# Optimization experiments

Hardware: AMD Instinct MI355X
Metric: run time of the kernel (lower is better)

## Reference

```python
import jax, jax.numpy as jnp
import numpy as np

B, T, C, H, D = 2, 2048, 1024, 16, 64

def setup_inputs() -> dict:
    key = jax.random.key(0)
    ks = jax.random.split(key, 5)
    s = 1.0 / np.sqrt(C)
    return {
        "hidden_states": jax.random.normal(ks[0], (B, T, C), jnp.float32),
        "Wq": jax.random.normal(ks[1], (H, C, D), jnp.float32) * s,
        "Wk": jax.random.normal(ks[2], (H, C, D), jnp.float32) * s,
        "Wv": jax.random.normal(ks[3], (H, C, D), jnp.float32) * s,
        "Wo": jax.random.normal(ks[4], (C, C), jnp.float32) * s,
    }

def reference(hidden_states, Wq, Wk, Wv, Wo):
    x = hidden_states  # (B, T, C)
    q = jnp.einsum("btc,hcd->bhtd", x, Wq)
    k = jnp.einsum("btc,hcd->bhtd", x, Wk)
    v = jnp.einsum("btc,hcd->bhtd", x, Wv)
    scale = 1.0 / jnp.sqrt(jnp.asarray(D, x.dtype))
    scores = jnp.einsum("bhtd,bhsd->bhts", q, k) * scale  # (B,H,T,T)
    Tlen = x.shape[1]
    causal = jnp.tril(jnp.ones((Tlen, Tlen), bool))
    scores = jnp.where(causal, scores, jnp.asarray(-jnp.inf, x.dtype))
    probs = jax.nn.softmax(scores, axis=-1)
    heads = jnp.einsum("bhts,bhsd->bhtd", probs, v)  # (B,H,T,D)
    concat = heads.transpose(0, 2, 1, 3).reshape(x.shape[0], Tlen, H * D)  # (B,T,C)
    return jnp.einsum("btc,oc->bto", concat, Wo)  # output projection (dropout=0)
```

## Files before the change

### kernel.cpp

```cpp
#include <hip/hip_runtime.h>
#include <math.h>

#define B_ 2
#define T_ 2048
#define C_ 1024
#define H_ 16
#define D_ 64

typedef short short8 __attribute__((ext_vector_type(8)));
typedef float f32x4 __attribute__((ext_vector_type(4)));
typedef float f32x16 __attribute__((ext_vector_type(16)));

#define LOG2E 1.44269504088896f

__device__ __forceinline__ unsigned short f2bf(float f) {
    unsigned int u = __float_as_uint(f);
    u += 0x7FFFu + ((u >> 16) & 1u);
    return (unsigned short)(u >> 16);
}

#define NCAST 2560

__global__ __launch_bounds__(256) void prep_all(
    const float* __restrict__ x,  const float* __restrict__ Wq,
    const float* __restrict__ Wk, const float* __restrict__ Wv,
    const float* __restrict__ Wo,
    unsigned short* __restrict__ xb,   unsigned short* __restrict__ Wall,
    unsigned short* __restrict__ wob,  int nX, int nW)
{
    const int bid = blockIdx.x;
    const int tid = threadIdx.x;
    if (bid < NCAST) {
        int i = (bid * 256 + tid) * 8;
        const float* s;
        unsigned short* d;
        if (i < nX) { s = x + i; d = xb + i; }
        else {
            int j = i - nX;
            if (j >= nW) return;
            s = Wo + j; d = wob + j;
        }
        float4 a = *(const float4*)s;
        float4 b = *(const float4*)(s + 4);
        ushort4 o0, o1;
        o0.x = f2bf(a.x); o0.y = f2bf(a.y); o0.z = f2bf(a.z); o0.w = f2bf(a.w);
        o1.x = f2bf(b.x); o1.y = f2bf(b.y); o1.z = f2bf(b.z); o1.w = f2bf(b.w);
        *(ushort4*)d = o0;
        *(ushort4*)(d + 4) = o1;
        return;
    }
    __shared__ float t[64][65];
    const int tb = bid - NCAST;
    const int c0 = (tb & 15) * 64;
    const int h  = (tb >> 4) & 15;
    const int z  = tb >> 8;
    const float* W = (z == 0) ? Wq : (z == 1) ? Wk : Wv;
    unsigned short* Wt = Wall + (size_t)z * H_ * D_ * C_;
    const int r = tid >> 4, c4 = (tid & 15) * 4;
    #pragma unroll
    for (int p = 0; p < 4; p++) {
        int cl = r + p * 16;
        float4 v = *(const float4*)&W[((size_t)h * C_ + c0 + cl) * D_ + c4];
        t[cl][c4 + 0] = v.x; t[cl][c4 + 1] = v.y;
        t[cl][c4 + 2] = v.z; t[cl][c4 + 3] = v.w;
    }
    __syncthreads();
    #pragma unroll
    for (int p = 0; p < 4; p++) {
        int d = r + p * 16;
        ushort4 o;
        o.x = f2bf(t[c4 + 0][d]); o.y = f2bf(t[c4 + 1][d]);
        o.z = f2bf(t[c4 + 2][d]); o.w = f2bf(t[c4 + 3][d]);
        *(ushort4*)&Wt[((size_t)h * D_ + d) * C_ + c0 + c4] = o;
    }
}

__global__ __launch_bounds__(256) void qkv_big(
    const unsigned short* __restrict__ X,
    const unsigned short* __restrict__ Wall,
    unsigned short* __restrict__ Qo,
    unsigned short* __restrict__ Ko,
    unsigned short* __restrict__ Vt)
{
    __shared__ unsigned short As[128][72];
    __shared__ unsigned short Bs[128][72];

    const int m0 = blockIdx.x * 128;
    const int n0 = blockIdx.y * 128;
    const int z  = n0 >> 10;
    const int tid = threadIdx.x;
    const int w = tid >> 6, lane = tid & 63, quad = lane >> 4, l16 = lane & 15;
    const int wm = w & 1, wn = w >> 1;
    const int lrow = tid >> 3, lcol = (tid & 7) * 8;

    f32x4 acc[4][4] = {};

    short8 ar[4], br[4];
    #pragma unroll
    for (int p = 0; p < 4; p++) {
        int r = lrow + p * 32;
        ar[p] = *(const short8*)&X[(size_t)(m0 + r) * C_ + lcol];
        br[p] = *(const short8*)&Wall[(size_t)(n0 + r) * C_ + lcol];
    }

    for (int k0 = 0; k0 < C_; k0 += 64) {
        __syncthreads();
        #pragma unroll
        for (int p = 0; p < 4; p++) {
            int r = lrow + p * 32;
            *(short8*)&As[r][lcol] = ar[p];
            *(short8*)&Bs[r][lcol] = br[p];
        }
        __syncthreads();
        if (k0 + 64 < C_) {
            #pragma unroll
            for (int p = 0; p < 4; p++) {
                int r = lrow + p * 32;
                ar[p] = *(const short8*)&X[(size_t)(m0 + r) * C_ + k0 + 64 + lcol];
                br[p] = *(const short8*)&Wall[(size_t)(n0 + r) * C_ + k0 + 64 + lcol];
            }
        }
        #pragma unroll
        for (int ks = 0; ks < 2; ks++) {
            short8 af[4], bf[4];
            #pragma unroll
            for (int i = 0; i < 4; i++)
                af[i] = *(const short8*)&As[wm * 64 + i * 16 + l16][ks * 32 + quad * 8];
            #pragma unroll
            for (int j = 0; j < 4; j++)
                bf[j] = *(const short8*)&Bs[wn * 64 + j * 16 + l16][ks * 32 + quad * 8];
            #pragma unroll
            for (int i = 0; i < 4; i++)
                #pragma unroll
                for (int j = 0; j < 4; j++)
                    acc[i][j] = __builtin_amdgcn_mfma_f32_16x16x32_bf16(af[i], bf[j], acc[i][j], 0, 0, 0);
        }
    }

    if (z == 2) {
        #pragma unroll
        for (int j = 0; j < 4; j++) {
            const int n = n0 + wn * 64 + j * 16 + l16;
            const int h = (n >> 6) & 15, d = n & 63;
            #pragma unroll
            for (int i = 0; i < 4; i++) {
                const int m = m0 + wm * 64 + i * 16 + quad * 4;
                const int b = m >> 11, t = m & (T_ - 1);
                ushort4 pk;
                pk.x = f2bf(acc[i][j][0]);
                pk.y = f2bf(acc[i][j][1]);
                pk.z = f2bf(acc[i][j][2]);
                pk.w = f2bf(acc[i][j][3]);
                *(ushort4*)&Vt[(((size_t)b * H_ + h) * D_ + d) * T_ + t] = pk;
            }
        }
    } else {
        const float scale = (z == 0) ? 0.125f * LOG2E : 1.0f;
        unsigned short* O = (z == 0) ? Qo : Ko;
        #pragma unroll
        for (int j = 0; j < 4; j++) {
            const int n = n0 + wn * 64 + j * 16 + l16;
            const int h = (n >> 6) & 15, d = n & 63;
            #pragma unroll
            for (int i = 0; i < 4; i++)
                #pragma unroll
                for (int r = 0; r < 4; r++) {
                    const int m = m0 + wm * 64 + i * 16 + quad * 4 + r;
                    const int b = m >> 11, t = m & (T_ - 1);
                    O[(((size_t)b * H_ + h) * T_ + t) * D_ + d] = f2bf(acc[i][j][r] * scale);
                }
        }
    }
}

__global__ __launch_bounds__(512, 4) void flash_mfma(
    const unsigned short* __restrict__ Q,
    const unsigned short* __restrict__ K,
    const unsigned short* __restrict__ Vt,
    unsigned short* __restrict__ CC)
{
    __shared__ unsigned short kst[64][72];
    __shared__ unsigned short vts[64][72];
    __shared__ float fob[2][64][68];
    __shared__ float flb_p[2][64];
    __shared__ float flb_t[2][64];

    const int dd   = blockIdx.x;
    const int xs   = dd & 7;
    const int loc  = dd >> 3;
    const int half = loc >> 5, li = loc & 31;
    const int hsub = li & 3, pr = li >> 2;
    const int p    = half ? (15 - pr) : pr;
    const int head = xs * 4 + hsub;
    const int h = head & 15, b = head >> 4;

    const int tid = threadIdx.x;
    const int w = tid >> 6, lane = tid & 63;
    const int l31 = lane & 31, hi = lane >> 5;
    const int wg = w & 3;
    const int g  = w >> 2;
    const int sw = (wg & 1) * 32;
    const int qw = (wg >> 1) * 32;
    const int lrow = tid >> 3, lcol = (tid & 7) * 8;
    const size_t hb  = ((size_t)b * H_ + h) * T_;
    const size_t hbD = ((size_t)b * H_ + h) * D_;

    const int qb  = g ? (31 - p) : p;
    const int q0  = qb * 64;
    const int myn = qb + 1;
    const int nkb = 32 - p;

    short8 qf[4];
    #pragma unroll
    for (int k4 = 0; k4 < 4; k4++)
        qf[k4] = *(const short8*)&Q[(hb + q0 + qw + l31) * D_ + k4 * 16 + hi * 8];

    float l_lane = 0.0f;
    f32x16 o0 = {}, o1 = {};

    short8 kreg, vreg;
    kreg = *(const short8*)&K[(hb + lrow) * D_ + lcol];
    vreg = *(const short8*)&Vt[(hbD + lrow) * T_ + lcol];

    for (int kb = 0; kb < nkb; kb++) {
        __syncthreads();
        *(short8*)&kst[lrow][lcol] = kreg;
        *(short8*)&vts[lrow][lcol] = vreg;
        __syncthreads();
        if (kb + 1 < nkb) {
            const int k0n = (kb + 1) * 64;
            kreg = *(const short8*)&K[(hb + k0n + lrow) * D_ + lcol];
            vreg = *(const short8*)&Vt[(hbD + lrow) * T_ + k0n + lcol];
        }

        if (kb < myn) {
            f32x16 S = {};
            __builtin_amdgcn_s_setprio(1);
            #pragma unroll
            for (int k4 = 0; k4 < 4; k4++) {
                short8 kf = *(const short8*)&kst[sw + l31][k4 * 16 + hi * 8];
                S = __builtin_amdgcn_mfma_f32_32x32x16_bf16(kf, qf[k4], S, 0, 0, 0);
            }
            __builtin_amdgcn_s_setprio(0);

            if (kb == qb) {
                #pragma unroll
                for (int reg = 0; reg < 16; reg++) {
                    const int srel = (reg & 3) + 4 * hi + 8 * (reg >> 2);
                    if (sw + srel > qw + l31) S[reg] = -INFINITY;
                }
            }

            unsigned Wd[8];
            #pragma unroll
            for (int blk = 0; blk < 4; blk++) {
                float e0 = exp2f(S[4 * blk + 0]);
                float e1 = exp2f(S[4 * blk + 1]);
                float e2 = exp2f(S[4 * blk + 2]);
                float e3 = exp2f(S[4 * blk + 3]);
                l_lane += (e0 + e1) + (e2 + e3);
                Wd[2 * blk + 0] = __builtin_amdgcn_perm(
                    __float_as_uint(e1) + 0x8000u, __float_as_uint(e0) + 0x8000u, 0x07060302u);
                Wd[2 * blk + 1] = __builtin_amdgcn_perm(
                    __float_as_uint(e3) + 0x8000u, __float_as_uint(e2) + 0x8000u, 0x07060302u);
            }

            unsigned a0 = Wd[0], b0 = Wd[2];
            asm("v_permlane32_swap_b32 %0, %1" : "+v"(a0), "+v"(b0));
            unsigned a1 = Wd[1], b1 = Wd[3];
            asm("v_permlane32_swap_b32 %0, %1" : "+v"(a1), "+v"(b1));
            unsigned c0 = Wd[4], d0 = Wd[6];
            asm("v_permlane32_swap_b32 %0, %1" : "+v"(c0), "+v"(d0));
            unsigned c1 = Wd[5], d1 = Wd[7];
            asm("v_permlane32_swap_b32 %0, %1" : "+v"(c1), "+v"(d1));
            union { unsigned u[4]; short8 v; } pw0, pw1;
            pw0.u[0] = a0; pw0.u[1] = a1; pw0.u[2] = b0; pw0.u[3] = b1;
            pw1.u[0] = c0; pw1.u[1] = c1; pw1.u[2] = d0; pw1.u[3] = d1;

            __builtin_amdgcn_s_setprio(1);
            {
                short8 vf;
                vf = *(const short8*)&vts[l31][sw + hi * 8];
                o0 = __builtin_amdgcn_mfma_f32_32x32x16_bf16(pw0.v, vf, o0, 0, 0, 0);
                vf = *(const short8*)&vts[l31][sw + 16 + hi * 8];
                o0 = __builtin_amdgcn_mfma_f32_32x32x16_bf16(pw1.v, vf, o0, 0, 0, 0);
                vf = *(const short8*)&vts[32 + l31][sw + hi * 8];
                o1 = __builtin_amdgcn_mfma_f32_32x32x16_bf16(pw0.v, vf, o1, 0, 0, 0);
                vf = *(const short8*)&vts[32 + l31][sw + 16 + hi * 8];
                o1 = __builtin_amdgcn_mfma_f32_32x32x16_bf16(pw1.v, vf, o1, 0, 0, 0);
            }
            __builtin_amdgcn_s_setprio(0);
        }
    }

    l_lane += __shfl_xor(l_lane, 32);

    if (wg & 1) {
        if (lane < 32) flb_p[g][qw + lane] = l_lane;
        #pragma unroll
        for (int reg = 0; reg < 16; reg++) {
            const int qr = (reg & 3) + 4 * hi + 8 * (reg >> 2);
            fob[g][qw + qr][l31]      = o0[reg];
            fob[g][qw + qr][32 + l31] = o1[reg];
        }
    }
    __syncthreads();
    if (!(wg & 1)) {
        const float lt = l_lane + flb_p[g][qw + l31];
        if (lane < 32) flb_t[g][qw + lane] = lt;
        #pragma unroll
        for (int reg = 0; reg < 16; reg++) {
            const int qr = (reg & 3) + 4 * hi + 8 * (reg >> 2);
            const float invl = 1.0f / flb_t[g][qw + qr];
            const float v0 = o0[reg] + fob[g][qw + qr][l31];
            const float v1 = o1[reg] + fob[g][qw + qr][32 + l31];
            const int t = q0 + qw + qr;
            CC[((size_t)b * T_ + t) * C_ + h * D_ + l31]      = f2bf(v0 * invl);
            CC[((size_t)b * T_ + t) * C_ + h * D_ + 32 + l31] = f2bf(v1 * invl);
        }
    }
}

__global__ __launch_bounds__(256) void out_big(
    const unsigned short* __restrict__ X,
    const unsigned short* __restrict__ Wob,
    float* __restrict__ out)
{
    __shared__ unsigned short As[128][72];
    __shared__ unsigned short Bs[128][72];

    const int m0 = blockIdx.x * 128;
    const int n0 = blockIdx.y * 128;
    const int tid = threadIdx.x;
    const int w = tid >> 6, lane = tid & 63, quad = lane >> 4, l16 = lane & 15;
    const int wm = w & 1, wn = w >> 1;
    const int lrow = tid >> 3, lcol = (tid & 7) * 8;

    f32x4 acc[4][4] = {};

    short8 ar[4], br[4];
    #pragma unroll
    for (int p = 0; p < 4; p++) {
        int r = lrow + p * 32;
        ar[p] = *(const short8*)&X[(size_t)(m0 + r) * C_ + lcol];
        br[p] = *(const short8*)&Wob[(size_t)(n0 + r) * C_ + lcol];
    }

    for (int k0 = 0; k0 < C_; k0 += 64) {
        __syncthreads();
        #pragma unroll
        for (int p = 0; p < 4; p++) {
            int r = lrow + p * 32;
            *(short8*)&As[r][lcol] = ar[p];
            *(short8*)&Bs[r][lcol] = br[p];
        }
        __syncthreads();
        if (k0 + 64 < C_) {
            #pragma unroll
            for (int p = 0; p < 4; p++) {
                int r = lrow + p * 32;
                ar[p] = *(const short8*)&X[(size_t)(m0 + r) * C_ + k0 + 64 + lcol];
                br[p] = *(const short8*)&Wob[(size_t)(n0 + r) * C_ + k0 + 64 + lcol];
            }
        }
        #pragma unroll
        for (int ks = 0; ks < 2; ks++) {
            short8 af[4], bf[4];
            #pragma unroll
            for (int i = 0; i < 4; i++)
                af[i] = *(const short8*)&As[wm * 64 + i * 16 + l16][ks * 32 + quad * 8];
            #pragma unroll
            for (int j = 0; j < 4; j++)
                bf[j] = *(const short8*)&Bs[wn * 64 + j * 16 + l16][ks * 32 + quad * 8];
            #pragma unroll
            for (int i = 0; i < 4; i++)
                #pragma unroll
                for (int j = 0; j < 4; j++)
                    acc[i][j] = __builtin_amdgcn_mfma_f32_16x16x32_bf16(af[i], bf[j], acc[i][j], 0, 0, 0);
        }
    }

    #pragma unroll
    for (int i = 0; i < 4; i++)
        #pragma unroll
        for (int j = 0; j < 4; j++)
            #pragma unroll
            for (int r = 0; r < 4; r++)
                out[(size_t)(m0 + wm * 64 + i * 16 + quad * 4 + r) * C_ + n0 + wn * 64 + j * 16 + l16] = acc[i][j][r];
}

extern "C" void kernel_launch(void* const* d_in, const int* in_sizes, int n_in,
                              void* d_out, int out_size, void* d_ws, size_t ws_size,
                              hipStream_t stream) {
    const float* x  = (const float*)d_in[0];
    const float* Wq = (const float*)d_in[1];
    const float* Wk = (const float*)d_in[2];
    const float* Wv = (const float*)d_in[3];
    const float* Wo = (const float*)d_in[4];
    float* out = (float*)d_out;

    const size_t nX = (size_t)B_ * T_ * C_;
    const size_t nW = (size_t)H_ * C_ * D_;
    const size_t nQ = (size_t)B_ * H_ * T_ * D_;
    unsigned short* xb   = (unsigned short*)d_ws;
    unsigned short* Wall = xb + nX;
    unsigned short* Wob  = Wall + 3 * nW;
    unsigned short* Qb   = Wob + nW;
    unsigned short* Kb   = Qb + nQ;
    unsigned short* Vtb  = Kb + nQ;
    unsigned short* CCb  = Vtb + nQ;

    prep_all<<<dim3(NCAST + 768), 256, 0, stream>>>(
        x, Wq, Wk, Wv, Wo, xb, Wall, Wob, (int)nX, (int)nW);
    qkv_big<<<dim3(32, 24), 256, 0, stream>>>(xb, Wall, Qb, Kb, Vtb);
    flash_mfma<<<dim3(512), 512, 0, stream>>>(Qb, Kb, Vtb, CCb);
    out_big<<<dim3(32, 8), 256, 0, stream>>>(CCb, Wob, out);
}
```

Baseline: 172.4 us.

## Rebalance causal flash workload between warp groups by splitting key blocks

The two 4-wave groups in each flash block previously handled a short query block p and a long query block 31-p, so group 0 idled for most of the loop. Now group 0 finishes its short block, switches to the long query block, and both groups process alternating key blocks, with two K/V tiles staged per step. Partial outputs and row sums are merged through shared memory in staged reductions at the end. This adds shared memory, extra register loads and more barriers in exchange for a shorter critical path per block.

Result: slower. 206.5 us (+19.8%).

```diff
diff --git a/kernel.cpp b/kernel.cpp
--- a/kernel.cpp
+++ b/kernel.cpp
@@ -179,8 +179,8 @@
     const unsigned short* __restrict__ Vt,
     unsigned short* __restrict__ CC)
 {
-    __shared__ unsigned short kst[64][72];
-    __shared__ unsigned short vts[64][72];
+    __shared__ unsigned short kst[128][72];
+    __shared__ unsigned short vts[128][72];
     __shared__ float fob[2][64][68];
     __shared__ float flb_p[2][64];
     __shared__ float flb_t[2][64];
@@ -205,45 +205,103 @@
     const size_t hb  = ((size_t)b * H_ + h) * T_;
     const size_t hbD = ((size_t)b * H_ + h) * D_;
 
-    const int qb  = g ? (31 - p) : p;
-    const int q0  = qb * 64;
-    const int myn = qb + 1;
-    const int nkb = 32 - p;
+    const int qbB = 31 - p;
+    const int p2s = p + 2;
+
+    int myqb = g ? qbB : p;
 
     short8 qf[4];
     #pragma unroll
     for (int k4 = 0; k4 < 4; k4++)
-        qf[k4] = *(const short8*)&Q[(hb + q0 + qw + l31) * D_ + k4 * 16 + hi * 8];
+        qf[k4] = *(const short8*)&Q[(hb + myqb * 64 + qw + l31) * D_ + k4 * 16 + hi * 8];
 
     float l_lane = 0.0f;
     f32x16 o0 = {}, o1 = {};
 
-    short8 kreg, vreg;
+    short8 kreg, vreg, kreg2, vreg2;
     kreg = *(const short8*)&K[(hb + lrow) * D_ + lcol];
     vreg = *(const short8*)&Vt[(hbD + lrow) * T_ + lcol];
 
-    for (int kb = 0; kb < nkb; kb++) {
+    for (int it = 0; it <= 16; it++) {
         __syncthreads();
         *(short8*)&kst[lrow][lcol] = kreg;
         *(short8*)&vts[lrow][lcol] = vreg;
+        if (it >= p2s) {
+            *(short8*)&kst[64 + lrow][lcol] = kreg2;
+            *(short8*)&vts[64 + lrow][lcol] = vreg2;
+        }
         __syncthreads();
-        if (kb + 1 < nkb) {
-            const int k0n = (kb + 1) * 64;
-            kreg = *(const short8*)&K[(hb + k0n + lrow) * D_ + lcol];
-            vreg = *(const short8*)&Vt[(hbD + lrow) * T_ + k0n + lcol];
-        }
-
-        if (kb < myn) {
+        if (it < 16) {
+            const int nit = it + 1;
+            if (nit < p2s) {
+                const int k0n = nit * 64;
+                kreg = *(const short8*)&K[(hb + k0n + lrow) * D_ + lcol];
+                vreg = *(const short8*)&Vt[(hbD + lrow) * T_ + k0n + lcol];
+            } else {
+                const int k0a = (p2s + 2 * (nit - p2s)) * 64;
+                kreg  = *(const short8*)&K[(hb + k0a + lrow) * D_ + lcol];
+                vreg  = *(const short8*)&Vt[(hbD + lrow) * T_ + k0a + lcol];
+                kreg2 = *(const short8*)&K[(hb + k0a + 64 + lrow) * D_ + lcol];
+                vreg2 = *(const short8*)&Vt[(hbD + lrow) * T_ + k0a + 64 + lcol];
+            }
+        }
+
+        if (g == 0 && it == p + 1) {
+            float lr = l_lane + __shfl_xor(l_lane, 32);
+            if (sw) {
+                if (lane < 32) flb_p[0][qw + lane] = lr;
+                #pragma unroll
+                for (int reg = 0; reg < 16; reg++) {
+                    const int qr = (reg & 3) + 4 * hi + 8 * (reg >> 2);
+                    fob[0][qw + qr][l31]      = o0[reg];
+                    fob[0][qw + qr][32 + l31] = o1[reg];
+                    o0[reg] = 0.0f; o1[reg] = 0.0f;
+                }
+                l_lane = 0.0f;
+            }
+            myqb = qbB;
+            #pragma unroll
+            for (int k4 = 0; k4 < 4; k4++)
+                qf[k4] = *(const short8*)&Q[(hb + qbB * 64 + qw + l31) * D_ + k4 * 16 + hi * 8];
+        }
+        if (g == 0 && !sw && it == p2s) {
+            float lr = l_lane + __shfl_xor(l_lane, 32);
+            float lt = lr + flb_p[0][qw + l31];
+            if (lane < 32) flb_t[0][qw + lane] = lt;
+            #pragma unroll
+            for (int reg = 0; reg < 16; reg++) {
+                const int qr = (reg & 3) + 4 * hi + 8 * (reg >> 2);
+                const float invl = 1.0f / flb_t[0][qw + qr];
+                const float v0 = o0[reg] + fob[0][qw + qr][l31];
+                const float v1 = o1[reg] + fob[0][qw + qr][32 + l31];
+                const int t = p * 64 + qw + qr;
+                CC[((size_t)b * T_ + t) * C_ + h * D_ + l31]      = f2bf(v0 * invl);
+                CC[((size_t)b * T_ + t) * C_ + h * D_ + 32 + l31] = f2bf(v1 * invl);
+                o0[reg] = 0.0f; o1[reg] = 0.0f;
+            }
+            l_lane = 0.0f;
+        }
+
+        bool active = true;
+        int kcur = it, rb = 0;
+        if (g == 0) {
+            if (it == p + 1)      active = false;
+            else if (it >= p2s)   kcur = p2s + 2 * (it - p2s);
+        } else {
+            if (it >= p2s)      { kcur = p2s + 2 * (it - p2s) + 1; rb = 64; }
+        }
+
+        if (active) {
             f32x16 S = {};
             __builtin_amdgcn_s_setprio(1);
             #pragma unroll
             for (int k4 = 0; k4 < 4; k4++) {
-                short8 kf = *(const short8*)&kst[sw + l31][k4 * 16 + hi * 8];
+                short8 kf = *(const short8*)&kst[rb + sw + l31][k4 * 16 + hi * 8];
                 S = __builtin_amdgcn_mfma_f32_32x32x16_bf16(kf, qf[k4], S, 0, 0, 0);
             }
             __builtin_amdgcn_s_setprio(0);
 
-            if (kb == qb) {
+            if (kcur == myqb) {
                 #pragma unroll
                 for (int reg = 0; reg < 16; reg++) {
                     const int srel = (reg & 3) + 4 * hi + 8 * (reg >> 2);
@@ -280,41 +338,81 @@
             __builtin_amdgcn_s_setprio(1);
             {
                 short8 vf;
-                vf = *(const short8*)&vts[l31][sw + hi * 8];
+                vf = *(const short8*)&vts[rb + l31][sw + hi * 8];
                 o0 = __builtin_amdgcn_mfma_f32_32x32x16_bf16(pw0.v, vf, o0, 0, 0, 0);
-                vf = *(const short8*)&vts[l31][sw + 16 + hi * 8];
+                vf = *(const short8*)&vts[rb + l31][sw + 16 + hi * 8];
                 o0 = __builtin_amdgcn_mfma_f32_32x32x16_bf16(pw1.v, vf, o0, 0, 0, 0);
-                vf = *(const short8*)&vts[32 + l31][sw + hi * 8];
+                vf = *(const short8*)&vts[rb + 32 + l31][sw + hi * 8];
                 o1 = __builtin_amdgcn_mfma_f32_32x32x16_bf16(pw0.v, vf, o1, 0, 0, 0);
-                vf = *(const short8*)&vts[32 + l31][sw + 16 + hi * 8];
+                vf = *(const short8*)&vts[rb + 32 + l31][sw + 16 + hi * 8];
                 o1 = __builtin_amdgcn_mfma_f32_32x32x16_bf16(pw1.v, vf, o1, 0, 0, 0);
             }
             __builtin_amdgcn_s_setprio(0);
         }
     }
 
-    l_lane += __shfl_xor(l_lane, 32);
-
-    if (wg & 1) {
-        if (lane < 32) flb_p[g][qw + lane] = l_lane;
+    __syncthreads();
+    if (g == 1 && sw) {
+        float lr = l_lane + __shfl_xor(l_lane, 32);
+        if (lane < 32) flb_p[1][qw + lane] = lr;
         #pragma unroll
         for (int reg = 0; reg < 16; reg++) {
             const int qr = (reg & 3) + 4 * hi + 8 * (reg >> 2);
-            fob[g][qw + qr][l31]      = o0[reg];
-            fob[g][qw + qr][32 + l31] = o1[reg];
-        }
-    }
-    __syncthreads();
-    if (!(wg & 1)) {
-        const float lt = l_lane + flb_p[g][qw + l31];
-        if (lane < 32) flb_t[g][qw + lane] = lt;
+            fob[1][qw + qr][l31]      = o0[reg];
+            fob[1][qw + qr][32 + l31] = o1[reg];
+        }
+    }
+    if (g == 0 && !sw && p == 15) {
+        float lr = l_lane + __shfl_xor(l_lane, 32);
+        float lt = lr + flb_p[0][qw + l31];
+        if (lane < 32) flb_t[0][qw + lane] = lt;
         #pragma unroll
         for (int reg = 0; reg < 16; reg++) {
             const int qr = (reg & 3) + 4 * hi + 8 * (reg >> 2);
-            const float invl = 1.0f / flb_t[g][qw + qr];
-            const float v0 = o0[reg] + fob[g][qw + qr][l31];
-            const float v1 = o1[reg] + fob[g][qw + qr][32 + l31];
-            const int t = q0 + qw + qr;
+            const float invl = 1.0f / flb_t[0][qw + qr];
+            const float v0 = o0[reg] + fob[0][qw + qr][l31];
+            const float v1 = o1[reg] + fob[0][qw + qr][32 + l31];
+            const int t = 15 * 64 + qw + qr;
+            CC[((size_t)b * T_ + t) * C_ + h * D_ + l31]      = f2bf(v0 * invl);
+            CC[((size_t)b * T_ + t) * C_ + h * D_ + 32 + l31] = f2bf(v1 * invl);
+            o0[reg] = 0.0f; o1[reg] = 0.0f;
+        }
+        l_lane = 0.0f;
+    }
+    __syncthreads();
+    if (g == 1 && !sw) {
+        float lr = l_lane + __shfl_xor(l_lane, 32);
+        if (lane < 32) flb_p[1][qw + lane] += lr;
+        #pragma unroll
+        for (int reg = 0; reg < 16; reg++) {
+            const int qr = (reg & 3) + 4 * hi + 8 * (reg >> 2);
+            fob[1][qw + qr][l31]      += o0[reg];
+            fob[1][qw + qr][32 + l31] += o1[reg];
+        }
+    }
+    __syncthreads();
+    if (g == 0 && sw) {
+        float lr = l_lane + __shfl_xor(l_lane, 32);
+        if (lane < 32) flb_p[1][qw + lane] += lr;
+        #pragma unroll
+        for (int reg = 0; reg < 16; reg++) {
+            const int qr = (reg & 3) + 4 * hi + 8 * (reg >> 2);
+            fob[1][qw + qr][l31]      += o0[reg];
+            fob[1][qw + qr][32 + l31] += o1[reg];
+        }
+    }
+    __syncthreads();
+    if (g == 0 && !sw) {
+        float lr = l_lane + __shfl_xor(l_lane, 32);
+        float lt = lr + flb_p[1][qw + l31];
+        if (lane < 32) flb_t[1][qw + lane] = lt;
+        #pragma unroll
+        for (int reg = 0; reg < 16; reg++) {
+            const int qr = (reg & 3) + 4 * hi + 8 * (reg >> 2);
+            const float invl = 1.0f / flb_t[1][qw + qr];
+            const float v0 = o0[reg] + fob[1][qw + qr][l31];
+            const float v1 = o1[reg] + fob[1][qw + qr][32 + l31];
+            const int t = qbB * 64 + qw + qr;
             CC[((size_t)b * T_ + t) * C_ + h * D_ + l31]      = f2bf(v0 * invl);
             CC[((size_t)b * T_ + t) * C_ + h * D_ + 32 + l31] = f2bf(v1 * invl);
         }
```
